# Optimization experiments

Measured on AMD Instinct MI355X. Metric: run time of the kernel, lower is better.

Reference implementation:

```python
import jax, jax.numpy as jnp
import numpy as np

N, K, D = 32768, 32, 128


def setup_inputs() -> dict:
    key = jax.random.key(0)
    ks = jax.random.split(key, 8)
    return {
        "x1": jax.random.normal(ks[0], (N, D), dtype=jnp.float32),
        "dists_argmax_1": jax.random.randint(ks[1], (N, K), 0, N),
        "dists_max_1": jax.random.uniform(ks[2], (N, K), dtype=jnp.float32),
        "x2": jax.random.normal(ks[3], (N, D), dtype=jnp.float32),
        "dists_argmax_2": jax.random.randint(ks[4], (N, K), 0, N),
        "dists_max_2": jax.random.uniform(ks[5], (N, K), dtype=jnp.float32),
        "w_out": jax.random.normal(ks[6], (1, D), dtype=jnp.float32) * (1.0 / np.sqrt(D)),
        "b_out": jnp.zeros((1,), dtype=jnp.float32),
    }


def _branch(x, idx, dmax, w_out, b_out):
    # anchor gather: [N,K,D]
    anchor = x[idx]
    # mcf 'default': distance-scaled anchor features (self_features unused)
    msgs = dmax[..., None] * anchor  # [N,K,D]
    # linear_out_position then squeeze(-1): [N,K]
    out_pos = jnp.einsum("nkd,d->nk", msgs, w_out[0]) + b_out[0]
    # agg 'mean' over anchor dim: [N,D]
    out_struct = jnp.mean(msgs, axis=1)
    return out_pos, out_struct


def reference(x1, dists_argmax_1, dists_max_1, x2, dists_argmax_2, dists_max_2, w_out, b_out):
    op1, os1 = _branch(x1, dists_argmax_1, dists_max_1, w_out, b_out)
    op2, os2 = _branch(x2, dists_argmax_2, dists_max_2, w_out, b_out)
    return (op1, os1, op2, os2)
```

## Files before the change

### kernel.cpp

```cpp
#include <hip/hip_runtime.h>

#define NN 32768
#define KK 32
#define DD 128

typedef float v2f __attribute__((ext_vector_type(2)));

__global__ __launch_bounds__(256) void prep_kernel(const float* __restrict__ x1,
                                                   const float* __restrict__ x2,
                                                   const float* __restrict__ w,
                                                   unsigned int* __restrict__ x8,
                                                   float* __restrict__ xw) {
    const int wave = threadIdx.x >> 6;
    const int lane = threadIdx.x & 63;
    const int half = lane >> 5;
    const int c    = lane & 31;
    const int row  = blockIdx.x * 8 + wave * 2 + half;
    const float* x = (row < NN) ? (x1 + (size_t)row * DD)
                                : (x2 + (size_t)(row - NN) * DD);
    const float4 xv = *(const float4*)(x + 4 * c);
    const float4 wv = *(const float4*)(w + 4 * c);

    int packed = __builtin_amdgcn_cvt_pk_fp8_f32(xv.x, xv.y, 0, false);
    packed     = __builtin_amdgcn_cvt_pk_fp8_f32(xv.z, xv.w, packed, true);
    x8[(size_t)row * 32 + c] = (unsigned int)packed;

    float s = xv.x * wv.x + xv.y * wv.y + xv.z * wv.z + xv.w * wv.w;
    #pragma unroll
    for (int m = 16; m >= 1; m >>= 1)
        s += __shfl_xor(s, m, 64);
    if (c == 0) xw[row] = s;
}

__global__ __launch_bounds__(256) void pgnn_main(
    const unsigned int* __restrict__ x8,
    const float*        __restrict__ xw,
    const int* __restrict__ idx1, const float* __restrict__ dm1,
    const int* __restrict__ idx2, const float* __restrict__ dm2,
    const float* __restrict__ b_out,
    float* __restrict__ out)
{
    const int branch = blockIdx.y;
    const unsigned int* __restrict__ xb  = x8 + (size_t)branch * NN * 32;
    const float*        __restrict__ xwb = xw + (size_t)branch * NN;
    const int*   __restrict__ idx = branch ? idx2 : idx1;
    const float* __restrict__ dm  = branch ? dm2  : dm1;
    float* __restrict__ op = out + (size_t)branch * ((size_t)NN * KK + (size_t)NN * DD);
    float* __restrict__ os = op + (size_t)NN * KK;

    __shared__ int   s_idx[8][KK];
    __shared__ float s_dm [8][KK];

    const int sub = threadIdx.x >> 5;
    const int c   = threadIdx.x & 31;
    const int n   = blockIdx.x * 8 + sub;

    const int   i  = idx[(size_t)n * KK + c];
    const float dv = dm [(size_t)n * KK + c];
    s_idx[sub][c] = i;
    s_dm [sub][c] = dv;
    op[(size_t)n * KK + c] = dv * xwb[i] + b_out[0];
    __syncthreads();

    float4 acc = make_float4(0.f, 0.f, 0.f, 0.f);
    #pragma unroll
    for (int k = 0; k < KK; ++k) {
        const int   r = s_idx[sub][k];
        const float d = s_dm [sub][k];
        const unsigned int u = xb[(size_t)r * 32 + c];
        const v2f f0 = __builtin_amdgcn_cvt_pk_f32_fp8((int)u, false);
        const v2f f1 = __builtin_amdgcn_cvt_pk_f32_fp8((int)u, true);
        acc.x += d * f0.x;
        acc.y += d * f0.y;
        acc.z += d * f1.x;
        acc.w += d * f1.y;
    }
    acc.x *= (1.0f / KK); acc.y *= (1.0f / KK);
    acc.z *= (1.0f / KK); acc.w *= (1.0f / KK);
    *(float4*)(os + (size_t)n * DD + 4 * c) = acc;
}

__global__ __launch_bounds__(256) void pgnn_fused(
    const float* __restrict__ x1, const int* __restrict__ idx1,
    const float* __restrict__ dm1,
    const float* __restrict__ x2, const int* __restrict__ idx2,
    const float* __restrict__ dm2,
    const float* __restrict__ w, const float* __restrict__ b_out,
    float* __restrict__ out)
{
    const int branch = blockIdx.y;
    const float* __restrict__ x   = branch ? x2   : x1;
    const int*   __restrict__ idx = branch ? idx2 : idx1;
    const float* __restrict__ dm  = branch ? dm2  : dm1;
    float* __restrict__ op = out + (size_t)branch * ((size_t)NN * KK + (size_t)NN * DD);
    float* __restrict__ os = op + (size_t)NN * KK;

    __shared__ int    s_idx[2][KK];
    __shared__ float  s_dm [2][KK];
    __shared__ float  s_dot[2][KK];
    __shared__ float4 s_acc[2][128];

    const int sub = threadIdx.x >> 7;
    const int t   = threadIdx.x & 127;
    const int g   = t >> 5;
    const int c   = t & 31;
    const int n   = blockIdx.x * 2 + sub;

    if (t < KK) {
        s_idx[sub][t] = idx[(size_t)n * KK + t];
        s_dm [sub][t] = dm [(size_t)n * KK + t];
    }
    const float4 wv = *(const float4*)(w + 4 * c);
    __syncthreads();

    float4 acc = make_float4(0.f, 0.f, 0.f, 0.f);
    #pragma unroll
    for (int k0 = 0; k0 < KK / 4; ++k0) {
        const int   kk  = k0 * 4 + g;
        const int   r   = s_idx[sub][kk];
        const float dmk = s_dm [sub][kk];
        const float4 v  = *(const float4*)(x + (size_t)r * DD + 4 * c);
        acc.x += dmk * v.x; acc.y += dmk * v.y;
        acc.z += dmk * v.z; acc.w += dmk * v.w;
        float p = v.x * wv.x + v.y * wv.y + v.z * wv.z + v.w * wv.w;
        #pragma unroll
        for (int m = 16; m >= 1; m >>= 1)
            p += __shfl_xor(p, m, 64);
        if (c == 0) s_dot[sub][kk] = p;
    }
    s_acc[sub][t] = acc;
    __syncthreads();

    if (t < KK)
        op[(size_t)n * KK + t] = s_dm[sub][t] * s_dot[sub][t] + b_out[0];
    if (t < 32) {
        const float4 a0 = s_acc[sub][t];
        const float4 a1 = s_acc[sub][32 + t];
        const float4 a2 = s_acc[sub][64 + t];
        const float4 a3 = s_acc[sub][96 + t];
        float4 r;
        r.x = (a0.x + a1.x + a2.x + a3.x) * (1.0f / KK);
        r.y = (a0.y + a1.y + a2.y + a3.y) * (1.0f / KK);
        r.z = (a0.z + a1.z + a2.z + a3.z) * (1.0f / KK);
        r.w = (a0.w + a1.w + a2.w + a3.w) * (1.0f / KK);
        *(float4*)(os + (size_t)n * DD + 4 * t) = r;
    }
}

extern "C" void kernel_launch(void* const* d_in, const int* in_sizes, int n_in,
                              void* d_out, int out_size, void* d_ws, size_t ws_size,
                              hipStream_t stream) {
    const float* x1   = (const float*)d_in[0];
    const int*   idx1 = (const int*)  d_in[1];
    const float* dm1  = (const float*)d_in[2];
    const float* x2   = (const float*)d_in[3];
    const int*   idx2 = (const int*)  d_in[4];
    const float* dm2  = (const float*)d_in[5];
    const float* w    = (const float*)d_in[6];
    const float* b    = (const float*)d_in[7];
    float* out = (float*)d_out;

    const size_t need = (size_t)2 * NN * DD
                      + (size_t)2 * NN * sizeof(float);
    if (ws_size >= need) {
        unsigned int* x8 = (unsigned int*)d_ws;
        float*        xw = (float*)((char*)d_ws + (size_t)2 * NN * DD);
        prep_kernel<<<dim3(2 * NN / 8), dim3(256), 0, stream>>>(x1, x2, w, x8, xw);
        pgnn_main<<<dim3(NN / 8, 2), dim3(256), 0, stream>>>(
            x8, xw, idx1, dm1, idx2, dm2, b, out);
    } else {
        pgnn_fused<<<dim3(NN / 2, 2), dim3(256), 0, stream>>>(
            x1, idx1, dm1, x2, idx2, dm2, w, b, out);
    }
}
```

Baseline: 133.1 us.

## Remap blocks to XCDs per branch, widen gathers, use nontemporal stores

Flattens the grid and maps block IDs so that each branch's blocks land on a fixed half of the eight XCDs. Each branch's FP8 feature table can then stay resident in those XCDs' L2 caches. Each block now handles 16 rows, with 16 threads per row each gathering 8 bytes (uint2), instead of 8 rows with 32 threads gathering 4 bytes. Outputs are written with nontemporal stores so they do not evict the gathered table from cache. The XCD mapping assumes round-robin dispatch of blocks across XCDs, and halving the threads per row doubles the per-thread work and accumulator registers.

```diff
diff --git a/kernel.cpp b/kernel.cpp
--- a/kernel.cpp
+++ b/kernel.cpp
@@ -5,6 +5,7 @@
 #define DD 128
 
 typedef float v2f __attribute__((ext_vector_type(2)));
+typedef float v4f __attribute__((ext_vector_type(4)));
 
 __global__ __launch_bounds__(256) void prep_kernel(const float* __restrict__ x1,
                                                    const float* __restrict__ x2,
@@ -33,51 +34,67 @@
 }
 
 __global__ __launch_bounds__(256) void pgnn_main(
-    const unsigned int* __restrict__ x8,
-    const float*        __restrict__ xw,
+    const uint2* __restrict__ x8,
+    const float* __restrict__ xw,
     const int* __restrict__ idx1, const float* __restrict__ dm1,
     const int* __restrict__ idx2, const float* __restrict__ dm2,
     const float* __restrict__ b_out,
     float* __restrict__ out)
 {
-    const int branch = blockIdx.y;
-    const unsigned int* __restrict__ xb  = x8 + (size_t)branch * NN * 32;
-    const float*        __restrict__ xwb = xw + (size_t)branch * NN;
+    const int g      = blockIdx.x;
+    const int xcd    = g & 7;
+    const int branch = xcd >> 2;
+    const int nb     = (g >> 3) * 4 + (xcd & 3);
+
+    const uint2* __restrict__ xb  = x8 + (size_t)branch * NN * 16;
+    const float* __restrict__ xwb = xw + (size_t)branch * NN;
     const int*   __restrict__ idx = branch ? idx2 : idx1;
     const float* __restrict__ dm  = branch ? dm2  : dm1;
     float* __restrict__ op = out + (size_t)branch * ((size_t)NN * KK + (size_t)NN * DD);
     float* __restrict__ os = op + (size_t)NN * KK;
 
-    __shared__ int   s_idx[8][KK];
-    __shared__ float s_dm [8][KK];
+    __shared__ int   s_idx[16][KK + 1];
+    __shared__ float s_dm [16][KK + 1];
 
-    const int sub = threadIdx.x >> 5;
-    const int c   = threadIdx.x & 31;
-    const int n   = blockIdx.x * 8 + sub;
+    const int tid = threadIdx.x;
+    const int n0  = nb * 16;
 
-    const int   i  = idx[(size_t)n * KK + c];
-    const float dv = dm [(size_t)n * KK + c];
-    s_idx[sub][c] = i;
-    s_dm [sub][c] = dv;
-    op[(size_t)n * KK + c] = dv * xwb[i] + b_out[0];
+    const float bb = b_out[0];
+    #pragma unroll
+    for (int j = tid; j < 16 * KK; j += 256) {
+        const int rr = j >> 5;
+        const int k  = j & 31;
+        const size_t off = (size_t)(n0 + rr) * KK + k;
+        const int   i  = idx[off];
+        const float dv = dm[off];
+        s_idx[rr][k] = i;
+        s_dm [rr][k] = dv;
+        __builtin_nontemporal_store(dv * xwb[i] + bb, &op[off]);
+    }
     __syncthreads();
 
-    float4 acc = make_float4(0.f, 0.f, 0.f, 0.f);
+    const int sub = tid >> 4;
+    const int h   = tid & 15;
+
+    float a0=0.f,a1=0.f,a2=0.f,a3=0.f,a4=0.f,a5=0.f,a6=0.f,a7=0.f;
     #pragma unroll
     for (int k = 0; k < KK; ++k) {
         const int   r = s_idx[sub][k];
         const float d = s_dm [sub][k];
-        const unsigned int u = xb[(size_t)r * 32 + c];
-        const v2f f0 = __builtin_amdgcn_cvt_pk_f32_fp8((int)u, false);
-        const v2f f1 = __builtin_amdgcn_cvt_pk_f32_fp8((int)u, true);
-        acc.x += d * f0.x;
-        acc.y += d * f0.y;
-        acc.z += d * f1.x;
-        acc.w += d * f1.y;
+        const uint2 u = xb[(size_t)r * 16 + h];
+        const v2f f0 = __builtin_amdgcn_cvt_pk_f32_fp8((int)u.x, false);
+        const v2f f1 = __builtin_amdgcn_cvt_pk_f32_fp8((int)u.x, true);
+        const v2f f2 = __builtin_amdgcn_cvt_pk_f32_fp8((int)u.y, false);
+        const v2f f3 = __builtin_amdgcn_cvt_pk_f32_fp8((int)u.y, true);
+        a0 += d * f0.x; a1 += d * f0.y; a2 += d * f1.x; a3 += d * f1.y;
+        a4 += d * f2.x; a5 += d * f2.y; a6 += d * f3.x; a7 += d * f3.y;
     }
-    acc.x *= (1.0f / KK); acc.y *= (1.0f / KK);
-    acc.z *= (1.0f / KK); acc.w *= (1.0f / KK);
-    *(float4*)(os + (size_t)n * DD + 4 * c) = acc;
+    const float inv = 1.0f / KK;
+    v4f o0 = { a0 * inv, a1 * inv, a2 * inv, a3 * inv };
+    v4f o1 = { a4 * inv, a5 * inv, a6 * inv, a7 * inv };
+    float* dst = os + (size_t)(n0 + sub) * DD + h * 8;
+    __builtin_nontemporal_store(o0, (v4f*)dst);
+    __builtin_nontemporal_store(o1, (v4f*)(dst + 4));
 }
 
 __global__ __launch_bounds__(256) void pgnn_fused(
@@ -102,7 +119,7 @@
 
     const int sub = threadIdx.x >> 7;
     const int t   = threadIdx.x & 127;
-    const int g   = t >> 5;
+    const int gg  = t >> 5;
     const int c   = t & 31;
     const int n   = blockIdx.x * 2 + sub;
 
@@ -116,7 +133,7 @@
     float4 acc = make_float4(0.f, 0.f, 0.f, 0.f);
     #pragma unroll
     for (int k0 = 0; k0 < KK / 4; ++k0) {
-        const int   kk  = k0 * 4 + g;
+        const int   kk  = k0 * 4 + gg;
         const int   r   = s_idx[sub][kk];
         const float dmk = s_dm [sub][kk];
         const float4 v  = *(const float4*)(x + (size_t)r * DD + 4 * c);
@@ -134,15 +151,15 @@
     if (t < KK)
         op[(size_t)n * KK + t] = s_dm[sub][t] * s_dot[sub][t] + b_out[0];
     if (t < 32) {
-        const float4 a0 = s_acc[sub][t];
-        const float4 a1 = s_acc[sub][32 + t];
-        const float4 a2 = s_acc[sub][64 + t];
-        const float4 a3 = s_acc[sub][96 + t];
+        const float4 b0 = s_acc[sub][t];
+        const float4 b1 = s_acc[sub][32 + t];
+        const float4 b2 = s_acc[sub][64 + t];
+        const float4 b3 = s_acc[sub][96 + t];
         float4 r;
-        r.x = (a0.x + a1.x + a2.x + a3.x) * (1.0f / KK);
-        r.y = (a0.y + a1.y + a2.y + a3.y) * (1.0f / KK);
-        r.z = (a0.z + a1.z + a2.z + a3.z) * (1.0f / KK);
-        r.w = (a0.w + a1.w + a2.w + a3.w) * (1.0f / KK);
+        r.x = (b0.x + b1.x + b2.x + b3.x) * (1.0f / KK);
+        r.y = (b0.y + b1.y + b2.y + b3.y) * (1.0f / KK);
+        r.z = (b0.z + b1.z + b2.z + b3.z) * (1.0f / KK);
+        r.w = (b0.w + b1.w + b2.w + b3.w) * (1.0f / KK);
         *(float4*)(os + (size_t)n * DD + 4 * t) = r;
     }
 }
@@ -166,8 +183,8 @@
         unsigned int* x8 = (unsigned int*)d_ws;
         float*        xw = (float*)((char*)d_ws + (size_t)2 * NN * DD);
         prep_kernel<<<dim3(2 * NN / 8), dim3(256), 0, stream>>>(x1, x2, w, x8, xw);
-        pgnn_main<<<dim3(NN / 8, 2), dim3(256), 0, stream>>>(
-            x8, xw, idx1, dm1, idx2, dm2, b, out);
+        pgnn_main<<<dim3(2 * NN / 16), dim3(256), 0, stream>>>(
+            (const uint2*)x8, xw, idx1, dm1, idx2, dm2, b, out);
     } else {
         pgnn_fused<<<dim3(NN / 2, 2), dim3(256), 0, stream>>>(
             x1, idx1, dm1, x2, idx2, dm2, w, b, out);
```

Result: no change. 134.0 us (+0.7%).
